# Kernel tuning notes

Measured on AMD Instinct MI355X. Metric: run time of the kernel, lower is better.

Reference implementation:

```python
import jax, jax.numpy as jnp
import numpy as np

B, S, H, K, E, C = 4, 1024, 1024, 8, 512, 10000

def setup_inputs() -> dict:
    key = jax.random.key(0)
    ks = jax.random.split(key, 5)
    context = jax.random.normal(ks[0], (B, S, H), dtype=jnp.float32)
    prior_w = jax.random.normal(ks[1], (K, H), dtype=jnp.float32) * 0.02
    prior_b = jnp.zeros((K,), dtype=jnp.float32)
    latent_w = jax.random.normal(ks[2], (K * E, H), dtype=jnp.float32) * 0.02
    latent_b = jnp.zeros((K * E,), dtype=jnp.float32)
    dec_w = jax.random.normal(ks[3], (C, E), dtype=jnp.float32) * 0.02
    dec_b = jnp.zeros((C,), dtype=jnp.float32)
    return {"context": context, "prior_w": prior_w, "prior_b": prior_b,
            "latent_w": latent_w, "latent_b": latent_b,
            "dec_w": dec_w, "dec_b": dec_b}

def reference(context, prior_w, prior_b, latent_w, latent_b, dec_w, dec_b):
    # priors: softmax over components  [B,S,K]
    priors = jax.nn.softmax(jnp.einsum('bsh,kh->bsk', context, prior_w) + prior_b, axis=-1)
    # latent: [B,S,K,E] after tanh (dropout is identity at inference, dropoutl=0)
    latent = jnp.tanh((jnp.einsum('bsh,eh->bse', context, latent_w) + latent_b)
                      .reshape(B, S, K, E))
    # decoder logits + per-component softmax over classes  [B,S,K,C]
    probs = jax.nn.softmax(jnp.einsum('bske,ce->bskc', latent, dec_w) + dec_b, axis=-1)
    # mixture-weighted sum over components  [B,S,C]
    return jnp.einsum('bsk,bskc->bsc', priors, probs)
```

## Files before the change

kernel.cpp:

```cpp
#include <hip/hip_runtime.h>
#include <hip/hip_bf16.h>


#define BM 128
#define BN 128
#define BK 64

typedef __attribute__((ext_vector_type(8))) short bf16x8;
typedef __attribute__((ext_vector_type(4))) float f32x4;
typedef __attribute__((ext_vector_type(8))) _Float16 f16x8;

typedef const __attribute__((address_space(1))) unsigned int* gas_u32p;
typedef __attribute__((address_space(3))) unsigned int* las_u32p;

__device__ __forceinline__ unsigned short f2bf(float x) {
  union { float f; unsigned int u; } un; un.f = x;
  unsigned int r = un.u + 0x7FFFu + ((un.u >> 16) & 1u);
  return (unsigned short)(r >> 16);
}

__global__ void k_cvt_bf16(const float4* __restrict__ src, ushort4* __restrict__ dst, int n4) {
  int i = blockIdx.x * blockDim.x + threadIdx.x;
  if (i < n4) {
    float4 v = src[i];
    ushort4 o;
    o.x = f2bf(v.x); o.y = f2bf(v.y); o.z = f2bf(v.z); o.w = f2bf(v.w);
    dst[i] = o;
  }
}

__global__ void k_priors(const float* __restrict__ ctx, const float* __restrict__ pw,
                         const float* __restrict__ pb, float* __restrict__ priors) {
  int t = blockIdx.x;
  int lane = threadIdx.x;
  __shared__ float logit[8];
  const float* c = ctx + (size_t)t * 1024;
  for (int k = 0; k < 8; ++k) {
    const float* w = pw + k * 1024;
    float s = 0.f;
    for (int h = lane; h < 1024; h += 64) s += c[h] * w[h];
    #pragma unroll
    for (int m = 1; m <= 32; m <<= 1) s += __shfl_xor(s, m);
    if (lane == 0) logit[k] = s + pb[k];
  }
  __syncthreads();
  if (lane == 0) {
    float mx = logit[0];
    for (int k = 1; k < 8; ++k) mx = fmaxf(mx, logit[k]);
    float z = 0.f, e[8];
    for (int k = 0; k < 8; ++k) { e[k] = __expf(logit[k] - mx); z += e[k]; }
    float inv = 1.f / z;
    for (int k = 0; k < 8; ++k) priors[(size_t)t * 8 + k] = e[k] * inv;
  }
}

__device__ __forceinline__ void gemm_mainloop(
    const unsigned short* __restrict__ A, const unsigned short* __restrict__ B,
    int lda, int ldb, int m0, int n0, int ktiles,
    unsigned short* ldsA, unsigned short* ldsB, f32x4 acc[4][4]) {
  const int tid = threadIdx.x;
  const int lane = tid & 63;
  const int wave = tid >> 6;
  const int wm = wave & 1, wn = wave >> 1;
  const int lrow = lane & 15, lq = lane >> 4;

  for (int kt = 0; kt < ktiles; ++kt) {
    int k0 = kt * BK;
    __syncthreads();
    #pragma unroll
    for (int p = 0; p < 4; ++p) {
      int chunk = p * 256 + tid;
      int row = chunk >> 3, kc = chunk & 7;
      int kcs = kc ^ (row & 7);
      __builtin_amdgcn_global_load_lds(
          (gas_u32p)(A + (size_t)(m0 + row) * lda + k0 + kcs * 8),
          (las_u32p)(ldsA + chunk * 8), 16, 0, 0);
      __builtin_amdgcn_global_load_lds(
          (gas_u32p)(B + (size_t)(n0 + row) * ldb + k0 + kcs * 8),
          (las_u32p)(ldsB + chunk * 8), 16, 0, 0);
    }
    __syncthreads();
    #pragma unroll
    for (int s = 0; s < 2; ++s) {
      int cbyteoff = (((s * 4 + lq) ^ (lrow & 7)) * 8);
      bf16x8 af[4], bfr[4];
      #pragma unroll
      for (int f = 0; f < 4; ++f)
        af[f] = *(const bf16x8*)(ldsA + (wm * 64 + f * 16 + lrow) * BK + cbyteoff);
      #pragma unroll
      for (int f = 0; f < 4; ++f)
        bfr[f] = *(const bf16x8*)(ldsB + (wn * 64 + f * 16 + lrow) * BK + cbyteoff);
      #pragma unroll
      for (int fi = 0; fi < 4; ++fi)
        #pragma unroll
        for (int fj = 0; fj < 4; ++fj)
          acc[fi][fj] = __builtin_amdgcn_mfma_f32_16x16x32_bf16(af[fi], bfr[fj], acc[fi][fj], 0, 0, 0);
    }
  }
}

__global__ __launch_bounds__(256, 4)
void k_latent(const unsigned short* __restrict__ ctxb, const unsigned short* __restrict__ lwb,
              const float* __restrict__ lb, unsigned short* __restrict__ latent) {
  __shared__ unsigned short lds[(BM + BN) * BK];
  f32x4 zero = {0.f, 0.f, 0.f, 0.f};
  f32x4 acc[4][4];
  #pragma unroll
  for (int i = 0; i < 4; ++i)
    #pragma unroll
    for (int j = 0; j < 4; ++j) acc[i][j] = zero;
  int l = blockIdx.x;
  int xcd = l & 7, idx = l >> 3;
  int ctl = idx & 3, by = idx >> 2;
  int m0 = by * BM, n0 = (xcd * 4 + ctl) * BN;
  gemm_mainloop(ctxb, lwb, 1024, 1024, m0, n0, 1024 / BK, lds, lds + BM * BK, acc);

  const int lane = threadIdx.x & 63, wave = threadIdx.x >> 6;
  const int wm = wave & 1, wn = wave >> 1, lrow = lane & 15, lq = lane >> 4;
  #pragma unroll
  for (int fi = 0; fi < 4; ++fi)
    #pragma unroll
    for (int fj = 0; fj < 4; ++fj) {
      int gcol = n0 + wn * 64 + fj * 16 + lrow;
      float bias = lb[gcol];
      #pragma unroll
      for (int r = 0; r < 4; ++r) {
        int grow = m0 + wm * 64 + fi * 16 + lq * 4 + r;
        float v = tanhf(acc[fi][fj][r] + bias);
        latent[(size_t)grow * 4096 + gcol] = f2bf(v);
      }
    }
}

template<int STORE>
__global__ __launch_bounds__(256, 4)
void k_dec_pass1(const unsigned short* __restrict__ latb, const unsigned short* __restrict__ dwb,
                 const float* __restrict__ db, float* __restrict__ Z,
                 _Float16* __restrict__ P) {
  __shared__ unsigned short lds[(BM + BN) * BK];
  int l = blockIdx.x;
  int xcd = l & 7, idx = l >> 3;
  int ctl = idx % 10, by = idx / 10;
  int n0 = (xcd * 10 + ctl) * BN, m0 = by * BM;
  if (n0 >= 10000) return;

  f32x4 zero = {0.f, 0.f, 0.f, 0.f};
  f32x4 acc[4][4];
  #pragma unroll
  for (int i = 0; i < 4; ++i)
    #pragma unroll
    for (int j = 0; j < 4; ++j) acc[i][j] = zero;
  gemm_mainloop(latb, dwb, 512, 512, m0, n0, 512 / BK, lds, lds + BM * BK, acc);

  const int lane = threadIdx.x & 63, wave = threadIdx.x >> 6;
  const int wm = wave & 1, wn = wave >> 1, lrow = lane & 15, lq = lane >> 4;

  if (STORE) __syncthreads();
  _Float16* ldsP = (_Float16*)lds;

  float rowsum[4][4];
  #pragma unroll
  for (int fi = 0; fi < 4; ++fi)
    #pragma unroll
    for (int r = 0; r < 4; ++r) rowsum[fi][r] = 0.f;
  #pragma unroll
  for (int fj = 0; fj < 4; ++fj) {
    int gcol = n0 + wn * 64 + fj * 16 + lrow;
    bool valid = gcol < 10000;
    float bias = valid ? db[gcol] : 0.f;
    #pragma unroll
    for (int fi = 0; fi < 4; ++fi)
      #pragma unroll
      for (int r = 0; r < 4; ++r) {
        float e = __expf(acc[fi][fj][r] + bias);
        if (STORE) {
          _Float16 h = (_Float16)e;
          if (valid) rowsum[fi][r] += (float)h;
          int row_l = wm * 64 + fi * 16 + lq * 4 + r;
          int col_l = wn * 64 + fj * 16 + lrow;
          ldsP[row_l * 128 + (((col_l >> 3) ^ (row_l & 7)) << 3) + (col_l & 7)] = h;
        } else {
          if (valid) rowsum[fi][r] += e;
        }
      }
  }

  if (STORE) {
    __syncthreads();
    #pragma unroll
    for (int it = 0; it < 8; ++it) {
      int chunk = it * 256 + threadIdx.x;
      int row_l = chunk >> 4, c8 = chunk & 15;
      int slot = c8 ^ (row_l & 7);
      uint4 v = *(const uint4*)((const char*)lds + row_l * 256 + slot * 16);
      *(uint4*)(P + (size_t)(m0 + row_l) * 10112 + n0 + c8 * 8) = v;
    }
  }

  #pragma unroll
  for (int fi = 0; fi < 4; ++fi)
    #pragma unroll
    for (int r = 0; r < 4; ++r) {
      float s = rowsum[fi][r];
      s += __shfl_xor(s, 1); s += __shfl_xor(s, 2);
      s += __shfl_xor(s, 4); s += __shfl_xor(s, 8);
      if (lrow == 0) atomicAdd(&Z[m0 + wm * 64 + fi * 16 + lq * 4 + r], s);
    }
}

__global__ __launch_bounds__(256)
void k_combine(const _Float16* __restrict__ P, const float* __restrict__ priors,
               const float* __restrict__ Z, float* __restrict__ out) {
  int t = blockIdx.x;
  const _Float16* base = P + (size_t)t * 8 * 10112;
  float w[8];
  #pragma unroll
  for (int k = 0; k < 8; ++k) w[k] = priors[t * 8 + k] / Z[t * 8 + k];
  for (int c8 = threadIdx.x; c8 < 1250; c8 += 256) {
    int c = c8 * 8;
    float s[8] = {0.f, 0.f, 0.f, 0.f, 0.f, 0.f, 0.f, 0.f};
    #pragma unroll
    for (int k = 0; k < 8; ++k) {
      f16x8 v = *(const f16x8*)(base + (size_t)k * 10112 + c);
      #pragma unroll
      for (int j = 0; j < 8; ++j) s[j] += w[k] * (float)v[j];
    }
    float4 o0 = {s[0], s[1], s[2], s[3]};
    float4 o1 = {s[4], s[5], s[6], s[7]};
    *(float4*)(out + (size_t)t * 10000 + c) = o0;
    *(float4*)(out + (size_t)t * 10000 + c + 4) = o1;
  }
}

__global__ __launch_bounds__(256, 4)
void k_dec_pass2(const unsigned short* __restrict__ latb, const unsigned short* __restrict__ dwb,
                 const float* __restrict__ db, const float* __restrict__ priors,
                 const float* __restrict__ Z, float* __restrict__ out) {
  __shared__ unsigned short lds[(BM + BN) * BK];
  int l = blockIdx.x;
  int xcd = l & 7, idx = l >> 3;
  int ctl = idx % 10, by = idx / 10;
  int n0 = (xcd * 10 + ctl) * BN, m0 = by * BM;
  if (n0 >= 10000) return;

  f32x4 zero = {0.f, 0.f, 0.f, 0.f};
  f32x4 acc[4][4];
  #pragma unroll
  for (int i = 0; i < 4; ++i)
    #pragma unroll
    for (int j = 0; j < 4; ++j) acc[i][j] = zero;
  gemm_mainloop(latb, dwb, 512, 512, m0, n0, 512 / BK, lds, lds + BM * BK, acc);

  const int tid = threadIdx.x;
  const int lane = tid & 63, wave = tid >> 6;
  const int wm = wave & 1, wn = wave >> 1, lrow = lane & 15, lq = lane >> 4;

  __syncthreads();
  float* ldsO = (float*)lds;

  #pragma unroll
  for (int fi = 0; fi < 4; ++fi) {
    int rbase = m0 + wm * 64 + fi * 16 + lq * 4;
    float w[4];
    #pragma unroll
    for (int r = 0; r < 4; ++r) w[r] = priors[rbase + r] / Z[rbase + r];
    #pragma unroll
    for (int fj = 0; fj < 4; ++fj) {
      int gcol = n0 + wn * 64 + fj * 16 + lrow;
      float bias = (gcol < 10000) ? db[gcol] : 0.f;
      float part = 0.f;
      #pragma unroll
      for (int r = 0; r < 4; ++r) part += w[r] * __expf(acc[fi][fj][r] + bias);
      float tok = part + __shfl_xor(part, 16);
      if (!(lq & 1)) {
        int tl = wm * 8 + fi * 2 + (lq >> 1);
        int cl = wn * 64 + fj * 16 + lrow;
        ldsO[tl * 128 + cl] = tok;
      }
    }
  }
  __syncthreads();
  int tok0 = m0 >> 3;
  #pragma unroll
  for (int it = 0; it < 2; ++it) {
    int f = it * 256 + tid;
    int tl = f >> 5, c4 = f & 31;
    int col = n0 + c4 * 4;
    if (col < 10000)
      *(float4*)(out + (size_t)(tok0 + tl) * 10000 + col) = *(float4*)(ldsO + tl * 128 + c4 * 4);
  }
}

extern "C" void kernel_launch(void* const* d_in, const int* in_sizes, int n_in,
                              void* d_out, int out_size, void* d_ws, size_t ws_size,
                              hipStream_t stream) {
  const float* ctx = (const float*)d_in[0];
  const float* pw  = (const float*)d_in[1];
  const float* pb  = (const float*)d_in[2];
  const float* lw  = (const float*)d_in[3];
  const float* lb  = (const float*)d_in[4];
  const float* dw  = (const float*)d_in[5];
  const float* db  = (const float*)d_in[6];
  float* out = (float*)d_out;

  char* ws = (char*)d_ws;
  unsigned short* ctxb = (unsigned short*)ws;
  unsigned short* lwb  = (unsigned short*)(ws + 8388608);
  unsigned short* dwb  = (unsigned short*)(ws + 16777216);
  unsigned short* latb = (unsigned short*)(ws + 27131904);
  float* priors        = (float*)(ws + 60686336);
  float* Z             = (float*)(ws + 60817408);
  _Float16* Pex        = (_Float16*)(ws + 60948480);
  const size_t WS_NEED_STORE = 60948480ull + 662700032ull;
  const bool store_path = ws_size >= WS_NEED_STORE;

  k_cvt_bf16<<<4096, 256, 0, stream>>>((const float4*)ctx, (ushort4*)ctxb, 1048576);
  k_cvt_bf16<<<4096, 256, 0, stream>>>((const float4*)lw,  (ushort4*)lwb,  1048576);
  k_cvt_bf16<<<5000, 256, 0, stream>>>((const float4*)dw,  (ushort4*)dwb,  1280000);
  hipMemsetAsync(dwb + (size_t)10000 * 512, 0, (size_t)112 * 512 * 2, stream);
  hipMemsetAsync(Z, 0, 32768 * 4, stream);

  k_priors<<<4096, 64, 0, stream>>>(ctx, pw, pb, priors);
  k_latent<<<1024, 256, 0, stream>>>(ctxb, lwb, lb, latb);
  if (store_path) {
    k_dec_pass1<1><<<20480, 256, 0, stream>>>(latb, dwb, db, Z, Pex);
    k_combine<<<4096, 256, 0, stream>>>(Pex, priors, Z, out);
  } else {
    k_dec_pass1<0><<<20480, 256, 0, stream>>>(latb, dwb, db, Z, nullptr);
    k_dec_pass2<<<20480, 256, 0, stream>>>(latb, dwb, db, priors, Z, out);
  }
}
```

Baseline: 1.115 ms.

## Chunk store path over row blocks so it fits smaller workspaces

Splits the decoder's store-probabilities path into row chunks sized to the available workspace, alternating pass1 and combine per chunk. This lets the cheaper store-and-combine path run instead of the recompute pass2 path whenever the workspace can hold at least an eighth of the rows. The combine kernel is also given a 2D grid so each block handles one 256-wide slice of classes instead of looping. Smaller chunks add launches and may keep the exchange buffer resident in cache, but reduce parallelism per launch.

Result: faster. 1.027 ms (-7.9%).

```diff
diff --git a/kernel.cpp b/kernel.cpp
--- a/kernel.cpp
+++ b/kernel.cpp
@@ -136,12 +136,12 @@
 __global__ __launch_bounds__(256, 4)
 void k_dec_pass1(const unsigned short* __restrict__ latb, const unsigned short* __restrict__ dwb,
                  const float* __restrict__ db, float* __restrict__ Z,
-                 _Float16* __restrict__ P) {
+                 _Float16* __restrict__ P, int m_base) {
   __shared__ unsigned short lds[(BM + BN) * BK];
   int l = blockIdx.x;
   int xcd = l & 7, idx = l >> 3;
   int ctl = idx % 10, by = idx / 10;
-  int n0 = (xcd * 10 + ctl) * BN, m0 = by * BM;
+  int n0 = (xcd * 10 + ctl) * BN, m0 = m_base + by * BM;
   if (n0 >= 10000) return;
 
   f32x4 zero = {0.f, 0.f, 0.f, 0.f};
@@ -193,7 +193,7 @@
       int row_l = chunk >> 4, c8 = chunk & 15;
       int slot = c8 ^ (row_l & 7);
       uint4 v = *(const uint4*)((const char*)lds + row_l * 256 + slot * 16);
-      *(uint4*)(P + (size_t)(m0 + row_l) * 10112 + n0 + c8 * 8) = v;
+      *(uint4*)(P + (size_t)(by * BM + row_l) * 10112 + n0 + c8 * 8) = v;
     }
   }
 
@@ -210,13 +210,15 @@
 
 __global__ __launch_bounds__(256)
 void k_combine(const _Float16* __restrict__ P, const float* __restrict__ priors,
-               const float* __restrict__ Z, float* __restrict__ out) {
-  int t = blockIdx.x;
-  const _Float16* base = P + (size_t)t * 8 * 10112;
+               const float* __restrict__ Z, float* __restrict__ out, int t_base) {
+  int tl = blockIdx.x;
+  int t  = t_base + tl;
+  const _Float16* base = P + (size_t)tl * 8 * 10112;
   float w[8];
   #pragma unroll
   for (int k = 0; k < 8; ++k) w[k] = priors[t * 8 + k] / Z[t * 8 + k];
-  for (int c8 = threadIdx.x; c8 < 1250; c8 += 256) {
+  int c8 = blockIdx.y * 256 + threadIdx.x;
+  if (c8 < 1250) {
     int c = c8 * 8;
     float s[8] = {0.f, 0.f, 0.f, 0.f, 0.f, 0.f, 0.f, 0.f};
     #pragma unroll
@@ -311,8 +313,14 @@
   float* priors        = (float*)(ws + 60686336);
   float* Z             = (float*)(ws + 60817408);
   _Float16* Pex        = (_Float16*)(ws + 60948480);
-  const size_t WS_NEED_STORE = 60948480ull + 662700032ull;
-  const bool store_path = ws_size >= WS_NEED_STORE;
+  const size_t WS_BASE = 60948480ull;
+
+  size_t avail = ws_size > WS_BASE ? ws_size - WS_BASE : 0;
+  long long mrows_ll = (long long)(avail / (10112ull * 2ull)) & ~127ll;
+  if (mrows_ll > 32768) mrows_ll = 32768;
+  int mrows = (int)mrows_ll;
+  int nch = mrows > 0 ? (32768 + mrows - 1) / mrows : 1000;
+  const bool store_path = (nch <= 8);
 
   k_cvt_bf16<<<4096, 256, 0, stream>>>((const float4*)ctx, (ushort4*)ctxb, 1048576);
   k_cvt_bf16<<<4096, 256, 0, stream>>>((const float4*)lw,  (ushort4*)lwb,  1048576);
@@ -323,10 +331,13 @@
   k_priors<<<4096, 64, 0, stream>>>(ctx, pw, pb, priors);
   k_latent<<<1024, 256, 0, stream>>>(ctxb, lwb, lb, latb);
   if (store_path) {
-    k_dec_pass1<1><<<20480, 256, 0, stream>>>(latb, dwb, db, Z, Pex);
-    k_combine<<<4096, 256, 0, stream>>>(Pex, priors, Z, out);
+    for (int ms = 0; ms < 32768; ms += mrows) {
+      int rows = 32768 - ms < mrows ? 32768 - ms : mrows;
+      k_dec_pass1<1><<<(rows / 128) * 80, 256, 0, stream>>>(latb, dwb, db, Z, Pex, ms);
+      k_combine<<<dim3(rows / 8, 5), 256, 0, stream>>>(Pex, priors, Z, out, ms / 8);
+    }
   } else {
-    k_dec_pass1<0><<<20480, 256, 0, stream>>>(latb, dwb, db, Z, nullptr);
+    k_dec_pass1<0><<<20480, 256, 0, stream>>>(latb, dwb, db, Z, nullptr, 0);
     k_dec_pass2<<<20480, 256, 0, stream>>>(latb, dwb, db, priors, Z, out);
   }
 }
```
